# Optimization experiments

Measured on AMD Instinct MI355X. Metric: run time of the kernel, lower is better.

The kernel has to match this reference:

```python
import jax, jax.numpy as jnp
import numpy as np
import math

NUM_EXPERTS = 16
MIN_EXPERTS_ACTIVE = 4  # num_experts // 4 for num_experts >= 8
WTH_MAX_C, WTH_ENTROPY_C, WTH_GAP_C = 0.4, 0.3, 0.3


def setup_inputs() -> dict:
    key = jax.random.key(0)
    k1, k2 = jax.random.split(key)
    N, C, H, W = 32768, 32, 8, 8
    patch = jax.random.normal(k1, (N, C, H, W), dtype=jnp.float32)
    keys = jax.random.normal(k2, (NUM_EXPERTS, C), dtype=jnp.float32)
    keys = keys / jnp.linalg.norm(keys, axis=-1, keepdims=True)  # keys are normalized centroids
    return {
        "patch": patch,
        "keys": keys,
        "logit_temp": jnp.float32(5.0),   # nn.Parameter init 5.0
        "mask_beta": jnp.float32(10.0),   # nn.Parameter init 10.0
        "threshold": jnp.float32(0.2),    # base routing threshold
    }


def _compute_gap(sort_weights):
    # sort_weights: [N, E] sorted descending; k = min(4, E-1)
    k = min(4, NUM_EXPERTS - 1)
    mean_rest = jnp.mean(sort_weights[:, 1:k + 1], axis=-1, keepdims=True)
    gap = (sort_weights[:, 0:1] - mean_rest) / (sort_weights[:, 0:1] + 1e-8)
    return jnp.clip(gap, 0.0, 1.0)


def _adaptive_threshold(weights, base_threshold):
    # weights: [N, E] softmax weights
    sort_weights = -jnp.sort(-weights, axis=-1)  # descending
    max_component = 1.0 - sort_weights[:, 0:1]
    mean_weight = jnp.mean(weights, axis=-1, keepdims=True)
    std_weight = jnp.std(weights, axis=-1, keepdims=True, ddof=1)  # torch unbiased std
    entropy = -jnp.sum(weights * jnp.log(weights + 1e-18), axis=-1, keepdims=True)
    entropy_component = 1.0 - entropy / math.log(NUM_EXPERTS)
    gap_component = _compute_gap(sort_weights)
    adaptive_factor = (WTH_MAX_C * max_component + WTH_ENTROPY_C * entropy_component
                       + WTH_GAP_C * gap_component)
    adaptive = base_threshold * (0.5 + adaptive_factor)
    min_thr = jnp.maximum(jnp.float32(0.05), mean_weight - 0.5 * std_weight)
    max_thr = jnp.minimum(jnp.float32(0.7), sort_weights[:, 0:1] - 0.1 * std_weight)
    # torch.clamp(x, min=a, max=b) == min(max(x, a), b)
    adaptive = jnp.minimum(jnp.maximum(adaptive, min_thr), max_thr)
    kth_weight = sort_weights[:, MIN_EXPERTS_ACTIVE - 1:MIN_EXPERTS_ACTIVE]
    adaptive = jnp.minimum(adaptive, kth_weight * 0.9)
    return adaptive


def reference(patch, keys, logit_temp, mask_beta, threshold):
    # SSP modeled as global average pooling over spatial dims -> [N, C]
    patch_emb = jnp.mean(patch, axis=(2, 3))
    # F.normalize(dim=-1): x / max(||x||, eps), eps = 1e-12
    norm = jnp.maximum(jnp.linalg.norm(patch_emb, axis=-1, keepdims=True), 1e-12)
    patch_emb = patch_emb / norm
    logits = patch_emb @ keys.T                      # [N, E]
    scaled_logits = logits / logit_temp + 1e-8
    weights = jax.nn.softmax(scaled_logits, axis=-1)
    adaptive_threshold = _adaptive_threshold(weights, threshold)
    # soft (default) masking path
    soft_mask = jax.nn.sigmoid((mask_beta + 1e-8) * (weights - adaptive_threshold))
    weights_filtered = weights * soft_mask
    sum_w = jnp.sum(weights_filtered, axis=-1, keepdims=True)
    weights_filtered = weights_filtered / jnp.maximum(sum_w, 1e-8)
    return weights_filtered
```

## Files before the change

### kernel.cpp

```cpp
#include <hip/hip_runtime.h>
#include <hip/hip_bf16.h>
#include <math.h>


#define C 32
#define HW 64
#define E 16
#define PPB 8
#define LOG_E16 2.7725887222397811f

__device__ __forceinline__ float rsum16(float x) {
    #pragma unroll
    for (int m = 1; m < 16; m <<= 1) x += __shfl_xor(x, m, 16);
    return x;
}
__device__ __forceinline__ float rmax16(float x) {
    #pragma unroll
    for (int m = 1; m < 16; m <<= 1) x = fmaxf(x, __shfl_xor(x, m, 16));
    return x;
}

__global__ __launch_bounds__(256) void router_kernel(
    const float* __restrict__ patch, const float* __restrict__ keys,
    const float* __restrict__ p_temp, const float* __restrict__ p_beta,
    const float* __restrict__ p_thr, float* __restrict__ out, int N)
{
    __shared__ float lds_emb[PPB * 33];
    __shared__ float lds_keys[E * 33];

    const int t = threadIdx.x;
    const int block0 = blockIdx.x * PPB;

    for (int i = t; i < E * C; i += 256)
        lds_keys[(i >> 5) * 33 + (i & 31)] = keys[i];

    const int p = t >> 5;
    const int c = t & 31;
    const int patch_idx = block0 + p;
    float emb = 0.0f;
    if (patch_idx < N) {
        const float4* base = (const float4*)patch + (size_t)patch_idx * (C * HW / 4) + c * (HW / 4);
        float4 acc = make_float4(0.f, 0.f, 0.f, 0.f);
        #pragma unroll
        for (int j = 0; j < HW / 4; ++j) {
            float4 v = base[j];
            acc.x += v.x; acc.y += v.y; acc.z += v.z; acc.w += v.w;
        }
        float mean = ((acc.x + acc.y) + (acc.z + acc.w)) * (1.0f / 64.0f);
        float sq = mean * mean;
        #pragma unroll
        for (int m = 1; m < 32; m <<= 1) sq += __shfl_xor(sq, m, 32);
        float inv = 1.0f / fmaxf(sqrtf(sq), 1e-12f);
        emb = mean * inv;
    }
    lds_emb[p * 33 + c] = emb;
    __syncthreads();

    if (t < PPB * E) {
        const int q = t >> 4;
        const int e = t & 15;
        const int pidx = block0 + q;
        if (pidx < N) {
            float logit = 0.0f;
            #pragma unroll
            for (int cc = 0; cc < C; ++cc)
                logit += lds_emb[q * 33 + cc] * lds_keys[e * 33 + cc];

            const float temp = p_temp[0];
            const float beta = p_beta[0];
            const float thr  = p_thr[0];

            float s = logit / temp + 1e-8f;

            float smax = rmax16(s);
            float ex = expf(s - smax);
            float esum = rsum16(ex);
            float w = ex / esum;

            float wsum = rsum16(w);
            float mean_w = wsum * (1.0f / 16.0f);
            float d = w - mean_w;
            float var = rsum16(d * d) * (1.0f / 15.0f);
            float std_w = sqrtf(var);
            float entropy = -rsum16(w * logf(w + 1e-18f));

            float v = w;
            const int lane16 = e;
            #pragma unroll
            for (int k = 2; k <= 16; k <<= 1) {
                #pragma unroll
                for (int j = k >> 1; j > 0; j >>= 1) {
                    float o = __shfl_xor(v, j, 16);
                    bool lower = (lane16 & j) == 0;
                    bool asc = (lane16 & k) != 0;
                    float lo = fminf(v, o), hi = fmaxf(v, o);
                    v = (asc == lower) ? lo : hi;
                }
            }
            float s0 = __shfl(v, 0, 16);
            float s1 = __shfl(v, 1, 16);
            float s2 = __shfl(v, 2, 16);
            float s3 = __shfl(v, 3, 16);
            float s4 = __shfl(v, 4, 16);

            float max_c = 1.0f - s0;
            float ent_c = 1.0f - entropy * (1.0f / LOG_E16);
            float mean_rest = 0.25f * ((s1 + s2) + (s3 + s4));
            float gap = (s0 - mean_rest) / (s0 + 1e-8f);
            gap = fminf(fmaxf(gap, 0.0f), 1.0f);
            float af = 0.4f * max_c + 0.3f * ent_c + 0.3f * gap;
            float adaptive = thr * (0.5f + af);
            float min_thr = fmaxf(0.05f, mean_w - 0.5f * std_w);
            float max_thr = fminf(0.7f, s0 - 0.1f * std_w);
            adaptive = fminf(fmaxf(adaptive, min_thr), max_thr);
            adaptive = fminf(adaptive, s3 * 0.9f);

            float z = (beta + 1e-8f) * (w - adaptive);
            float mask = 1.0f / (1.0f + expf(-z));
            float wf = w * mask;
            float sw = rsum16(wf);
            wf = wf / fmaxf(sw, 1e-8f);

            out[(size_t)pidx * E + e] = wf;
        }
    }
}

extern "C" void kernel_launch(void* const* d_in, const int* in_sizes, int n_in,
                              void* d_out, int out_size, void* d_ws, size_t ws_size,
                              hipStream_t stream) {
    const float* patch = (const float*)d_in[0];
    const float* keys  = (const float*)d_in[1];
    const float* lt    = (const float*)d_in[2];
    const float* mb    = (const float*)d_in[3];
    const float* th    = (const float*)d_in[4];
    float* out = (float*)d_out;
    int N = in_sizes[0] / (C * HW);
    int blocks = (N + PPB - 1) / PPB;
    router_kernel<<<blocks, 256, 0, stream>>>(patch, keys, lt, mb, th, out, N);
}
```

Baseline: 365.0 us.

## Coalesce patch loads across wave lanes and double patches per block

Each wave now handles four patches, and its lanes read consecutive float4s so global loads are fully coalesced. Previously each thread read its own strided 256-byte channel row. Channel means are reduced with 16-lane shuffles and the norm with a 64-lane shuffle, and the normalization is applied to the logits afterwards. Blocks now cover 16 patches, so all 256 threads take part in the routing phase. The cost is more shuffle work per load.

```diff
diff --git a/kernel.cpp b/kernel.cpp
--- a/kernel.cpp
+++ b/kernel.cpp
@@ -6,7 +6,8 @@
 #define C 32
 #define HW 64
 #define E 16
-#define PPB 8
+#define PPW 4
+#define PPB 16
 #define LOG_E16 2.7725887222397811f
 
 __device__ __forceinline__ float rsum16(float x) {
@@ -19,6 +20,11 @@
     for (int m = 1; m < 16; m <<= 1) x = fmaxf(x, __shfl_xor(x, m, 16));
     return x;
 }
+__device__ __forceinline__ float rsum64(float x) {
+    #pragma unroll
+    for (int m = 1; m < 64; m <<= 1) x += __shfl_xor(x, m, 64);
+    return x;
+}
 
 __global__ __launch_bounds__(256) void router_kernel(
     const float* __restrict__ patch, const float* __restrict__ keys,
@@ -26,45 +32,52 @@
     const float* __restrict__ p_thr, float* __restrict__ out, int N)
 {
     __shared__ float lds_emb[PPB * 33];
+    __shared__ float lds_inv[PPB];
     __shared__ float lds_keys[E * 33];
 
     const int t = threadIdx.x;
+    const int wave = t >> 6;
+    const int lane = t & 63;
     const int block0 = blockIdx.x * PPB;
 
     for (int i = t; i < E * C; i += 256)
         lds_keys[(i >> 5) * 33 + (i & 31)] = keys[i];
 
-    const int p = t >> 5;
-    const int c = t & 31;
-    const int patch_idx = block0 + p;
-    float emb = 0.0f;
-    if (patch_idx < N) {
-        const float4* base = (const float4*)patch + (size_t)patch_idx * (C * HW / 4) + c * (HW / 4);
-        float4 acc = make_float4(0.f, 0.f, 0.f, 0.f);
-        #pragma unroll
-        for (int j = 0; j < HW / 4; ++j) {
-            float4 v = base[j];
-            acc.x += v.x; acc.y += v.y; acc.z += v.z; acc.w += v.w;
+    #pragma unroll
+    for (int pp = 0; pp < PPW; ++pp) {
+        const int p = wave * PPW + pp;
+        const int pidx = block0 + p;
+        if (pidx < N) {
+            const float4* base = (const float4*)(patch + (size_t)pidx * (C * HW));
+            float sq = 0.0f;
+            #pragma unroll
+            for (int j = 0; j < 8; ++j) {
+                float4 v = base[j * 64 + lane];
+                float s = ((v.x + v.y) + (v.z + v.w));
+                s = rsum16(s);
+                float mean = s * (1.0f / 64.0f);
+                sq += mean * mean;
+                if ((lane & 15) == 0)
+                    lds_emb[p * 33 + j * 4 + (lane >> 4)] = mean;
+            }
+            float tot = rsum64(sq) * (1.0f / 16.0f);
+            float inv = 1.0f / fmaxf(sqrtf(tot), 1e-12f);
+            if (lane == 0) lds_inv[p] = inv;
         }
-        float mean = ((acc.x + acc.y) + (acc.z + acc.w)) * (1.0f / 64.0f);
-        float sq = mean * mean;
-        #pragma unroll
-        for (int m = 1; m < 32; m <<= 1) sq += __shfl_xor(sq, m, 32);
-        float inv = 1.0f / fmaxf(sqrtf(sq), 1e-12f);
-        emb = mean * inv;
     }
-    lds_emb[p * 33 + c] = emb;
     __syncthreads();
 
-    if (t < PPB * E) {
+    {
         const int q = t >> 4;
         const int e = t & 15;
         const int pidx = block0 + q;
         if (pidx < N) {
+            const float inv = lds_inv[q];
             float logit = 0.0f;
             #pragma unroll
             for (int cc = 0; cc < C; ++cc)
                 logit += lds_emb[q * 33 + cc] * lds_keys[e * 33 + cc];
+            logit *= inv;
 
             const float temp = p_temp[0];
             const float beta = p_beta[0];
```

Measured after the change: 364.3 us. Within noise of the previous version (-0.2%).
